# Kernel optimization log

Hardware: AMD Instinct MI355X
Metric: run time of the kernel (lower is better)

## Reference

```python
import jax, jax.numpy as jnp
import numpy as np

NEG_SLOPE = 0.2
EPS_SOFTMAX = 1e-16
EPS_NORM = 1e-12
H = 4


def gat_conv(x, src, dst, edge_attr, W, att_src, att_dst, W_edge, att_edge, bias, concat):
    """PyG GATConv with edge_dim, add_self_loops=False.
    x: [N, F_in]; src,dst: [E]; edge_attr: [E, edge_dim]
    W: [F_in, H*C]; att_src/att_dst/att_edge: [H, C]; W_edge: [edge_dim, H*C]
    """
    N = x.shape[0]
    C = att_src.shape[1]
    xs = (x @ W).reshape(N, H, C)                      # [N,H,C]
    a_s = jnp.einsum('nhc,hc->nh', xs, att_src)        # [N,H]
    a_d = jnp.einsum('nhc,hc->nh', xs, att_dst)        # [N,H]
    e = (edge_attr @ W_edge).reshape(-1, H, C)         # [E,H,C]
    a_e = jnp.einsum('ehc,hc->eh', e, att_edge)        # [E,H]
    alpha = a_s[src] + a_d[dst] + a_e                  # [E,H]
    alpha = jax.nn.leaky_relu(alpha, NEG_SLOPE)
    # segment softmax over edges grouped by destination node
    m = jax.ops.segment_max(alpha, dst, num_segments=N)        # [N,H]
    ex = jnp.exp(alpha - m[dst])
    denom = jax.ops.segment_sum(ex, dst, num_segments=N)       # [N,H]
    alpha = ex / (denom[dst] + EPS_SOFTMAX)
    # message = attention-weighted source features, scatter-add to dst
    out = jax.ops.segment_sum(xs[src] * alpha[..., None], dst, num_segments=N)  # [N,H,C]
    out = out.reshape(N, H * C) if concat else out.mean(axis=1)
    return out + bias


def l2_normalize(x):
    n = jnp.linalg.norm(x, axis=-1, keepdims=True)
    return x / jnp.maximum(n, EPS_NORM)


def setup_inputs() -> dict:
    key = jax.random.key(0)
    ks = jax.random.split(key, 16)
    N, E, F_in, C1, C2 = 50000, 800000, 128, 64, 64
    glorot = lambda k, shape: jax.random.uniform(
        k, shape, jnp.float32, -1.0, 1.0) * np.sqrt(6.0 / (shape[0] + shape[-1]))
    return {
        'x': jax.random.normal(ks[0], (N, F_in), jnp.float32),
        'edge_index': jax.random.randint(ks[1], (2, E), 0, N, jnp.int32),
        'edge_weight': jax.random.uniform(ks[2], (E, 1), jnp.float32),
        # layer 1: in=128 -> H*C1=256, concat=True
        'W1': glorot(ks[3], (F_in, H * C1)),
        'att_src1': glorot(ks[4], (H, C1)),
        'att_dst1': glorot(ks[5], (H, C1)),
        'We1': glorot(ks[6], (1, H * C1)),
        'att_e1': glorot(ks[7], (H, C1)),
        'b1': jnp.zeros((H * C1,), jnp.float32),
        # layer 2: in=256 -> H*C2, concat=False (mean over heads)
        'W2': glorot(ks[8], (H * C1, H * C2)),
        'att_src2': glorot(ks[9], (H, C2)),
        'att_dst2': glorot(ks[10], (H, C2)),
        'We2': glorot(ks[11], (1, H * C2)),
        'att_e2': glorot(ks[12], (H, C2)),
        'b2': jnp.zeros((C2,), jnp.float32),
    }


def reference(x, edge_index, edge_weight, W1, att_src1, att_dst1, We1, att_e1, b1,
              W2, att_src2, att_dst2, We2, att_e2, b2):
    src, dst = edge_index[0], edge_index[1]
    h = gat_conv(x, src, dst, edge_weight, W1, att_src1, att_dst1, We1, att_e1, b1, concat=True)
    h = jax.nn.relu(l2_normalize(h))
    out = gat_conv(h, src, dst, edge_weight, W2, att_src2, att_dst2, We2, att_e2, b2, concat=False)
    return out
```

## Files before the change

kernel.cpp:

```cpp
#include <hip/hip_runtime.h>
#include <hip/hip_bf16.h>

typedef unsigned short u16;
typedef unsigned long long u64;
using bf16x8 = __attribute__((ext_vector_type(8))) short;
using f32x4v = __attribute__((ext_vector_type(4))) float;
typedef float v2f __attribute__((ext_vector_type(2)));

#define HC 256
#define CDIM 64

__device__ __forceinline__ float b2f(u16 u){
  union { unsigned int i; float f; } c; c.i = ((unsigned)u) << 16; return c.f;
}
__device__ __forceinline__ u16 f2b(float f){
  union { float f; unsigned int i; } c; c.f = f;
  unsigned int x = c.i;
  return (u16)((x + 0x7FFFu + ((x >> 16) & 1u)) >> 16);
}
__device__ __forceinline__ float ldf(const void* p, size_t i, int isbf){
  return isbf ? b2f(((const u16*)p)[i]) : ((const float*)p)[i];
}
__device__ __forceinline__ float sel4(float4 v, int h){ return h==0?v.x:(h==1?v.y:(h==2?v.z:v.w)); }
__device__ __forceinline__ float lrelu(float v){ return v>0.f ? v : 0.2f*v; }

__device__ __forceinline__ void glds16(const void* g, void* l){
  __builtin_amdgcn_global_load_lds(
      (const __attribute__((address_space(1))) unsigned int*)g,
      (__attribute__((address_space(3))) unsigned int*)l, 16, 0, 0);
}

__device__ __forceinline__ float4 wave_max4(float4 m){
  #pragma unroll
  for(int o=32;o>0;o>>=1){
    m.x=fmaxf(m.x,__shfl_xor(m.x,o));
    m.y=fmaxf(m.y,__shfl_xor(m.y,o));
    m.z=fmaxf(m.z,__shfl_xor(m.z,o));
    m.w=fmaxf(m.w,__shfl_xor(m.w,o));
  }
  return m;
}
__device__ __forceinline__ float4 wave_sum4(float4 m){
  #pragma unroll
  for(int o=32;o>0;o>>=1){
    m.x+=__shfl_xor(m.x,o);
    m.y+=__shfl_xor(m.y,o);
    m.z+=__shfl_xor(m.z,o);
    m.w+=__shfl_xor(m.w,o);
  }
  return m;
}

__global__ void k_hist(const int* __restrict__ dst, int E, int N, int* __restrict__ deg,
                       int* __restrict__ rank,
                       const u16* __restrict__ x, int nelem, int* __restrict__ flag){
  int e = blockIdx.x*256 + threadIdx.x;
  if (e < E){
    int d = dst[e];
    if ((unsigned)d < (unsigned)N) rank[e] = atomicAdd(&deg[d], 1);
  }
  if (blockIdx.x == 0){
    __shared__ int bad;
    if (threadIdx.x==0) bad = 0;
    __syncthreads();
    int n = nelem < 8192 ? nelem : 8192;
    int localbad = 0;
    for (int i=threadIdx.x; i<n; i+=256){
      int ex = (x[i] >> 7) & 0xFF;
      if (ex >= 140) localbad++;
    }
    if (localbad) atomicAdd(&bad, 1);
    __syncthreads();
    if (threadIdx.x==0) *flag = (bad==0) ? 1 : 0;
  }
}

__global__ void k_scan1(const int* __restrict__ in, int* __restrict__ out, int* __restrict__ bsums, int n){
  __shared__ int s[256];
  int t = threadIdx.x;
  int i = blockIdx.x*256 + t;
  int v = (i<n)? in[i] : 0;
  s[t]=v; __syncthreads();
  for(int off=1; off<256; off<<=1){
    int tv = (t>=off)? s[t-off] : 0;
    __syncthreads();
    s[t]+=tv; __syncthreads();
  }
  if (i<n) out[i] = s[t]-v;
  if (t==255) bsums[blockIdx.x] = s[255];
}

__global__ void k_scan2(int* __restrict__ bsums, int nb){
  __shared__ int s[256];
  int t=threadIdx.x;
  int v=(t<nb)? bsums[t]:0;
  s[t]=v; __syncthreads();
  for(int off=1; off<256; off<<=1){
    int tv=(t>=off)? s[t-off]:0;
    __syncthreads();
    s[t]+=tv; __syncthreads();
  }
  if (t<nb) bsums[t]=s[t]-v;
}

__global__ void k_scatter(const int* __restrict__ src, const int* __restrict__ dst,
                          const void* __restrict__ ew, int E, int N,
                          const int* __restrict__ rowptr, const int* __restrict__ bsums,
                          const int* __restrict__ rank, u64* __restrict__ epk,
                          const int* __restrict__ flagp){
  int e = blockIdx.x*256+threadIdx.x;
  if (e>=E) return;
  int bf = *flagp;
  int d = dst[e];
  if ((unsigned)d >= (unsigned)N) return;
  int p = rowptr[d] + bsums[d>>8] + rank[e];
  int s = src[e];
  if ((unsigned)s >= (unsigned)N) s = 0;
  u64 v = ((u64)__float_as_uint(ldf(ew, e, bf)) << 32) | (unsigned)s;
  __builtin_nontemporal_store(v, &epk[p]);
}

__global__ void k_prep(const void* __restrict__ W1, const void* __restrict__ W2,
                       const void* __restrict__ We1, const void* __restrict__ ae1,
                       const void* __restrict__ We2, const void* __restrict__ ae2,
                       u16* __restrict__ Bt1, u16* __restrict__ Bt2, float* __restrict__ ce,
                       const int* __restrict__ flagp){
  int bf = *flagp;
  int b = blockIdx.x, t = threadIdx.x;
  if (b < 128){
    Bt1[(size_t)t*128 + b] = f2b(ldf(W1, (size_t)b*HC + t, bf));
  } else if (b < 384){
    int k = b - 128;
    Bt2[(size_t)t*256 + k] = f2b(ldf(W2, (size_t)k*HC + t, bf));
  } else {
    float p1 = ldf(We1, t, bf)*ldf(ae1, t, bf);
    float p2 = ldf(We2, t, bf)*ldf(ae2, t, bf);
    #pragma unroll
    for(int o=32;o>0;o>>=1){ p1+=__shfl_xor(p1,o); p2+=__shfl_xor(p2,o); }
    if((t&63)==0){ ce[t>>6]=p1; ce[4+(t>>6)]=p2; }
  }
}

__global__ __launch_bounds__(256) void k_gemm_mfma(
    const void* __restrict__ A, int a_ext, const u16* __restrict__ Bt,
    u16* __restrict__ C, const void* __restrict__ att_s, const void* __restrict__ att_d,
    float* __restrict__ a_s, float* __restrict__ a_d,
    int M, int K, const int* __restrict__ flagp)
{
  __shared__ u16 sh[64*264];
  __shared__ float att_sh[512];
  u16* As = sh;
  u16* Bs = sh + 2048;
  int bf = *flagp;
  int a_bf = a_ext ? bf : 1;
  int tid = threadIdx.x;
  int lane = tid & 63, w = tid >> 6;
  int quad = lane >> 4, ln = lane & 15;
  int m0 = blockIdx.x * 64;

  att_sh[tid]       = ldf(att_s, tid, bf);
  att_sh[256 + tid] = ldf(att_d, tid, bf);

  f32x4v acc[4][4] = {};
  for (int k0 = 0; k0 < K; k0 += 32){
    if (!a_ext){
      const u16* gA = (const u16*)A + (size_t)(m0 + (tid>>2))*K + k0 + (size_t)(tid&3)*8;
      glds16(gA, (char*)As + (size_t)w*1024);
    } else {
      int m = tid >> 2, g = tid & 3;
      int r = m0 + m;
      uint4 pack;
      if (r < M){
        size_t base = (size_t)r*K + k0 + g*8;
        if (a_bf){
          pack = *(const uint4*)((const u16*)A + base);
        } else {
          const float* Af = (const float*)A + base;
          float4 f0 = *(const float4*)Af;
          float4 f1 = *(const float4*)(Af+4);
          unsigned a0 = (unsigned)f2b(f0.x) | ((unsigned)f2b(f0.y)<<16);
          unsigned a1 = (unsigned)f2b(f0.z) | ((unsigned)f2b(f0.w)<<16);
          unsigned a2 = (unsigned)f2b(f1.x) | ((unsigned)f2b(f1.y)<<16);
          unsigned a3 = (unsigned)f2b(f1.z) | ((unsigned)f2b(f1.w)<<16);
          pack = make_uint4(a0,a1,a2,a3);
        }
      } else pack = make_uint4(0,0,0,0);
      ((uint4*)As)[tid] = pack;
    }
    #pragma unroll
    for (int i=0;i<4;i++){
      const u16* gB = Bt + (size_t)(i*64 + (tid>>2))*K + k0 + (size_t)(tid&3)*8;
      glds16(gB, (char*)Bs + (size_t)i*4096 + (size_t)w*1024);
    }
    __syncthreads();
    bf16x8 af[4], bfr[4];
    #pragma unroll
    for (int mi=0;mi<4;mi++) af[mi] = *(const bf16x8*)&As[(mi*16+ln)*32 + quad*8];
    #pragma unroll
    for (int nj=0;nj<4;nj++) bfr[nj] = *(const bf16x8*)&Bs[((size_t)w*64+nj*16+ln)*32 + quad*8];
    #pragma unroll
    for (int mi=0;mi<4;mi++)
      #pragma unroll
      for (int nj=0;nj<4;nj++)
        acc[mi][nj] = __builtin_amdgcn_mfma_f32_16x16x32_bf16(af[mi], bfr[nj], acc[mi][nj], 0,0,0);
    __syncthreads();
  }
  #pragma unroll
  for (int mi=0;mi<4;mi++)
    #pragma unroll
    for (int nj=0;nj<4;nj++){
      union { __hip_bfloat162 h2; u16 u[2]; } cv0, cv1;
      cv0.h2 = __float22bfloat162_rn(make_float2(acc[mi][nj][0], acc[mi][nj][1]));
      cv1.h2 = __float22bfloat162_rn(make_float2(acc[mi][nj][2], acc[mi][nj][3]));
      int col = w*64 + nj*16 + ln;
      int rbase = mi*16 + quad*4;
      sh[(rbase+0)*264 + col] = cv0.u[0];
      sh[(rbase+1)*264 + col] = cv0.u[1];
      sh[(rbase+2)*264 + col] = cv1.u[0];
      sh[(rbase+3)*264 + col] = cv1.u[1];
    }
  __syncthreads();
  #pragma unroll
  for (int j=0;j<8;j++){
    int idx = j*256 + tid;
    int r = idx >> 5, gq = idx & 31;
    if (m0 + r < M)
      *(uint4*)(C + (size_t)(m0+r)*HC + gq*8) = *(const uint4*)&sh[r*264 + gq*8];
  }
  {
    int r  = w*16 + ln;
    int hh = quad;
    const u16* crow = &sh[r*264 + hh*64];
    const float* asv = &att_sh[hh*64];
    const float* adv = &att_sh[256 + hh*64];
    float ps = 0.f, pd = 0.f;
    #pragma unroll
    for (int cb=0; cb<64; cb+=8){
      ushort4 ua = *(const ushort4*)&crow[cb];
      ushort4 ub = *(const ushort4*)&crow[cb+4];
      float4 sa = *(const float4*)&asv[cb];
      float4 sb = *(const float4*)&asv[cb+4];
      float4 da = *(const float4*)&adv[cb];
      float4 db = *(const float4*)&adv[cb+4];
      float c0=b2f(ua.x), c1=b2f(ua.y), c2=b2f(ua.z), c3=b2f(ua.w);
      float c4=b2f(ub.x), c5=b2f(ub.y), c6=b2f(ub.z), c7=b2f(ub.w);
      ps += c0*sa.x + c1*sa.y + c2*sa.z + c3*sa.w + c4*sb.x + c5*sb.y + c6*sb.z + c7*sb.w;
      pd += c0*da.x + c1*da.y + c2*da.z + c3*da.w + c4*db.x + c5*db.y + c6*db.z + c7*db.w;
    }
    if (m0 + r < M){
      a_s[(size_t)(m0+r)*4 + hh] = ps;
      a_d[(size_t)(m0+r)*4 + hh] = pd;
    }
  }
}

#define GRP4(E0, TWJ) { \
  int s0_=__builtin_amdgcn_readlane(s_reg,(E0)+0); \
  int s1_=__builtin_amdgcn_readlane(s_reg,(E0)+1); \
  int s2_=__builtin_amdgcn_readlane(s_reg,(E0)+2); \
  int s3_=__builtin_amdgcn_readlane(s_reg,(E0)+3); \
  uint2 x0_=*(const uint2*)&xs[(size_t)s0_*HC + (lane<<2)]; \
  uint2 x1_=*(const uint2*)&xs[(size_t)s1_*HC + (lane<<2)]; \
  uint2 x2_=*(const uint2*)&xs[(size_t)s2_*HC + (lane<<2)]; \
  uint2 x3_=*(const uint2*)&xs[(size_t)s3_*HC + (lane<<2)]; \
  float w0_=__shfl((TWJ), ibase+(((E0)+0)&15)); \
  float w1_=__shfl((TWJ), ibase+(((E0)+1)&15)); \
  float w2_=__shfl((TWJ), ibase+(((E0)+2)&15)); \
  float w3_=__shfl((TWJ), ibase+(((E0)+3)&15)); \
  v2f f_; \
  f_=(v2f){__uint_as_float(x0_.x<<16),__uint_as_float(x0_.x&0xFFFF0000u)}; a01+=f_*w0_; \
  f_=(v2f){__uint_as_float(x0_.y<<16),__uint_as_float(x0_.y&0xFFFF0000u)}; a23+=f_*w0_; \
  f_=(v2f){__uint_as_float(x1_.x<<16),__uint_as_float(x1_.x&0xFFFF0000u)}; a01+=f_*w1_; \
  f_=(v2f){__uint_as_float(x1_.y<<16),__uint_as_float(x1_.y&0xFFFF0000u)}; a23+=f_*w1_; \
  f_=(v2f){__uint_as_float(x2_.x<<16),__uint_as_float(x2_.x&0xFFFF0000u)}; a01+=f_*w2_; \
  f_=(v2f){__uint_as_float(x2_.y<<16),__uint_as_float(x2_.y&0xFFFF0000u)}; a23+=f_*w2_; \
  f_=(v2f){__uint_as_float(x3_.x<<16),__uint_as_float(x3_.x&0xFFFF0000u)}; a01+=f_*w3_; \
  f_=(v2f){__uint_as_float(x3_.y<<16),__uint_as_float(x3_.y&0xFFFF0000u)}; a23+=f_*w3_; \
}

__global__ __launch_bounds__(256) void k_soft_agg(
    const u16* __restrict__ xs, const int* __restrict__ rowptr, const int* __restrict__ bsums,
    const int* __restrict__ deg, const u64* __restrict__ epk,
    const float* __restrict__ a_s, const float* __restrict__ a_d, const float* __restrict__ ce4,
    const void* __restrict__ bias, void* __restrict__ outp, int N, int layer,
    const int* __restrict__ flagp){
  int bf = *flagp;
  int lane = threadIdx.x & 63;
  int w = threadIdx.x >> 6;
  int n = (blockIdx.x<<2) + w;
  if (n >= N) return;
  int row = rowptr[n] + bsums[n>>8];
  int dg = deg[n];
  float4 ad = *(const float4*)&a_d[(size_t)n*4];
  float4 ce = *(const float4*)ce4;
  int h = lane >> 4;
  float4 acc = make_float4(0.f,0.f,0.f,0.f);
  if (dg > 0){
    if (dg <= 64){
      u64 pk = 0;
      if (lane < dg) pk = epk[row + lane];
      int s = (int)(unsigned)(pk & 0xFFFFFFFFull);
      if ((unsigned)s >= (unsigned)N) s = 0;
      int s_reg = s;
      float wv = __uint_as_float((unsigned)(pk >> 32));
      float4 as4 = *(const float4*)&a_s[(size_t)s*4];
      uint2 xpf[8];
      #pragma unroll
      for (int k=0;k<8;k++){
        int sk = __builtin_amdgcn_readlane(s_reg, k);
        xpf[k] = *(const uint2*)&xs[(size_t)sk*HC + (lane<<2)];
      }
      bool vlane = lane < dg;
      float4 ex;
      ex.x = vlane ? __expf(lrelu(as4.x+ad.x+wv*ce.x)) : 0.f;
      ex.y = vlane ? __expf(lrelu(as4.y+ad.y+wv*ce.y)) : 0.f;
      ex.z = vlane ? __expf(lrelu(as4.z+ad.z+wv*ce.z)) : 0.f;
      ex.w = vlane ? __expf(lrelu(as4.w+ad.w+wv*ce.w)) : 0.f;
      float4 ss = ex;
      if (dg > 32){
        ss.x+=__shfl_xor(ss.x,32); ss.y+=__shfl_xor(ss.y,32);
        ss.z+=__shfl_xor(ss.z,32); ss.w+=__shfl_xor(ss.w,32);
      }
      if (dg > 16){
        ss.x+=__shfl_xor(ss.x,16); ss.y+=__shfl_xor(ss.y,16);
        ss.z+=__shfl_xor(ss.z,16); ss.w+=__shfl_xor(ss.w,16);
      }
      #pragma unroll
      for(int o=8;o>0;o>>=1){
        ss.x+=__shfl_xor(ss.x,o); ss.y+=__shfl_xor(ss.y,o);
        ss.z+=__shfl_xor(ss.z,o); ss.w+=__shfl_xor(ss.w,o);
      }
      float4 wgt;
      wgt.x = ex.x/(ss.x+1e-16f); wgt.y = ex.y/(ss.y+1e-16f);
      wgt.z = ex.z/(ss.z+1e-16f); wgt.w = ex.w/(ss.w+1e-16f);
      int ibase = lane & 48;
      float tw0, tw1, tw2, tw3;
      {
        int srcl = lane & 15;
        float c0=__shfl(wgt.x,srcl), c1=__shfl(wgt.y,srcl);
        float c2=__shfl(wgt.z,srcl), c3=__shfl(wgt.w,srcl);
        tw0 = (h==0)?c0:((h==1)?c1:((h==2)?c2:c3));
      }
      if (dg > 16){
        int srcl = 16 + (lane & 15);
        float c0=__shfl(wgt.x,srcl), c1=__shfl(wgt.y,srcl);
        float c2=__shfl(wgt.z,srcl), c3=__shfl(wgt.w,srcl);
        tw1 = (h==0)?c0:((h==1)?c1:((h==2)?c2:c3));
      } else tw1 = 0.f;
      if (dg > 32){
        int srcl = 32 + (lane & 15);
        float c0=__shfl(wgt.x,srcl), c1=__shfl(wgt.y,srcl);
        float c2=__shfl(wgt.z,srcl), c3=__shfl(wgt.w,srcl);
        tw2 = (h==0)?c0:((h==1)?c1:((h==2)?c2:c3));
      } else tw2 = 0.f;
      if (dg > 48){
        int srcl = 48 + (lane & 15);
        float c0=__shfl(wgt.x,srcl), c1=__shfl(wgt.y,srcl);
        float c2=__shfl(wgt.z,srcl), c3=__shfl(wgt.w,srcl);
        tw3 = (h==0)?c0:((h==1)?c1:((h==2)?c2:c3));
      } else tw3 = 0.f;
      v2f a01 = {0.f,0.f}, a23 = {0.f,0.f};
      #pragma unroll
      for (int k=0;k<8;k++){
        float wk = __shfl(tw0, ibase+k);
        uint2 xv = xpf[k];
        v2f f;
        f = (v2f){__uint_as_float(xv.x<<16), __uint_as_float(xv.x&0xFFFF0000u)}; a01 += f*wk;
        f = (v2f){__uint_as_float(xv.y<<16), __uint_as_float(xv.y&0xFFFF0000u)}; a23 += f*wk;
      }
      if (dg >  8) GRP4( 8, tw0);
      if (dg > 12) GRP4(12, tw0);
      if (dg > 16){
        GRP4(16, tw1);
        if (dg > 20) GRP4(20, tw1);
        if (dg > 24) GRP4(24, tw1);
        if (dg > 28) GRP4(28, tw1);
        if (dg > 32){
          GRP4(32, tw2);
          if (dg > 36) GRP4(36, tw2);
          if (dg > 40) GRP4(40, tw2);
          if (dg > 44) GRP4(44, tw2);
          if (dg > 48){
            GRP4(48, tw3);
            if (dg > 52) GRP4(52, tw3);
            if (dg > 56) GRP4(56, tw3);
            if (dg > 60) GRP4(60, tw3);
          }
        }
      }
      acc.x = a01.x; acc.y = a01.y; acc.z = a23.x; acc.w = a23.y;
    } else {
      float4 m = make_float4(-1e30f,-1e30f,-1e30f,-1e30f);
      for (int p=lane;p<dg;p+=64){
        u64 pk = epk[row+p];
        int s = (int)(unsigned)(pk & 0xFFFFFFFFull);
        if ((unsigned)s >= (unsigned)N) s = 0;
        float wv = __uint_as_float((unsigned)(pk >> 32));
        float4 as = *(const float4*)&a_s[(size_t)s*4];
        m.x=fmaxf(m.x, lrelu(as.x+ad.x+wv*ce.x));
        m.y=fmaxf(m.y, lrelu(as.y+ad.y+wv*ce.y));
        m.z=fmaxf(m.z, lrelu(as.z+ad.z+wv*ce.z));
        m.w=fmaxf(m.w, lrelu(as.w+ad.w+wv*ce.w));
      }
      m = wave_max4(m);
      float4 ss = make_float4(0.f,0.f,0.f,0.f);
      for (int p=lane;p<dg;p+=64){
        u64 pk = epk[row+p];
        int s = (int)(unsigned)(pk & 0xFFFFFFFFull);
        if ((unsigned)s >= (unsigned)N) s = 0;
        float wv = __uint_as_float((unsigned)(pk >> 32));
        float4 as = *(const float4*)&a_s[(size_t)s*4];
        ss.x+=__expf(lrelu(as.x+ad.x+wv*ce.x)-m.x);
        ss.y+=__expf(lrelu(as.y+ad.y+wv*ce.y)-m.y);
        ss.z+=__expf(lrelu(as.z+ad.z+wv*ce.z)-m.z);
        ss.w+=__expf(lrelu(as.w+ad.w+wv*ce.w)-m.w);
      }
      ss = wave_sum4(ss);
      float rsel=1.f/(sel4(ss,h)+1e-16f), mh=sel4(m,h), adh=sel4(ad,h), ceh=sel4(ce,h);
      for (int e=0;e<dg;e++){
        u64 pk = epk[row+e];
        int s = (int)(unsigned)(pk & 0xFFFFFFFFull);
        if ((unsigned)s >= (unsigned)N) s = 0;
        float wv = __uint_as_float((unsigned)(pk >> 32));
        float arv = lrelu(a_s[(size_t)s*4+h]+adh+wv*ceh);
        float wgt = __expf(arv-mh)*rsel;
        ushort4 xv4 = *(const ushort4*)&xs[(size_t)s*HC + lane*4];
        acc.x+=wgt*b2f(xv4.x); acc.y+=wgt*b2f(xv4.y);
        acc.z+=wgt*b2f(xv4.z); acc.w+=wgt*b2f(xv4.w);
      }
    }
  }
  if (layer==1){
    float4 v;
    v.x = acc.x + ldf(bias, lane*4+0, bf);
    v.y = acc.y + ldf(bias, lane*4+1, bf);
    v.z = acc.z + ldf(bias, lane*4+2, bf);
    v.w = acc.w + ldf(bias, lane*4+3, bf);
    float ss = v.x*v.x+v.y*v.y+v.z*v.z+v.w*v.w;
    #pragma unroll
    for(int o=32;o>0;o>>=1) ss += __shfl_xor(ss,o);
    float inv = 1.f/fmaxf(sqrtf(ss), 1e-12f);
    ushort4 o4;
    o4.x = f2b(fmaxf(v.x*inv,0.f)); o4.y = f2b(fmaxf(v.y*inv,0.f));
    o4.z = f2b(fmaxf(v.z*inv,0.f)); o4.w = f2b(fmaxf(v.w*inv,0.f));
    *(ushort4*)((u16*)outp + (size_t)n*HC + lane*4) = o4;
  } else {
    float4 s = acc;
    #pragma unroll
    for (int o=16;o<=32;o<<=1){
      s.x+=__shfl_xor(s.x,o); s.y+=__shfl_xor(s.y,o);
      s.z+=__shfl_xor(s.z,o); s.w+=__shfl_xor(s.w,o);
    }
    if (lane < 16){
      float4 v;
      v.x = 0.25f*s.x + ldf(bias, lane*4+0, bf);
      v.y = 0.25f*s.y + ldf(bias, lane*4+1, bf);
      v.z = 0.25f*s.z + ldf(bias, lane*4+2, bf);
      v.w = 0.25f*s.w + ldf(bias, lane*4+3, bf);
      if (bf){
        ushort4 o4; o4.x=f2b(v.x); o4.y=f2b(v.y); o4.z=f2b(v.z); o4.w=f2b(v.w);
        *(ushort4*)((u16*)outp + (size_t)n*CDIM + lane*4) = o4;
      } else {
        *(float4*)((float*)outp + (size_t)n*CDIM + lane*4) = v;
      }
    }
  }
}

extern "C" void kernel_launch(void* const* d_in, const int* in_sizes, int n_in,
                              void* d_out, int out_size, void* d_ws, size_t ws_size,
                              hipStream_t stream){
  const void* x_in = d_in[0];
  const int* eidx  = (const int*)d_in[1];
  const void* ew   = d_in[2];
  const void* W1   = d_in[3];
  const void* as1  = d_in[4];
  const void* ad1  = d_in[5];
  const void* We1  = d_in[6];
  const void* ae1  = d_in[7];
  const void* b1   = d_in[8];
  const void* W2   = d_in[9];
  const void* as2  = d_in[10];
  const void* ad2  = d_in[11];
  const void* We2  = d_in[12];
  const void* ae2  = d_in[13];
  const void* b2   = d_in[14];

  int N = in_sizes[0]/128;
  int E = in_sizes[2];
  const int* src = eidx;
  const int* dst = eidx + E;

  char* w = (char*)d_ws;
  auto alloc = [&](size_t bytes)->char*{ char* p=w; w += (bytes+255)/256*256; return p; };
  int*   flag  = (int*)alloc(256);
  u16*   xs    = (u16*)alloc((size_t)N*HC*2);
  u16*   agg   = (u16*)alloc((size_t)N*HC*2);
  float* a_s   = (float*)alloc((size_t)N*4*4);
  float* a_d   = (float*)alloc((size_t)N*4*4);
  int*   deg   = (int*)alloc((size_t)N*4);
  int*   rowptr= (int*)alloc((size_t)N*4);
  int*   bsums = (int*)alloc(256*4);
  int*   rank  = (int*)alloc((size_t)E*4);
  u64*   epk   = (u64*)alloc((size_t)E*8);
  float* ce    = (float*)alloc(256);
  u16*   Bt1   = (u16*)alloc((size_t)HC*128*2);
  u16*   Bt2   = (u16*)alloc((size_t)HC*HC*2);

  (void)hipMemsetAsync(deg, 0, (size_t)N*4, stream);

  int eb = (E+255)/256;
  int nb = (N+255)/256;
  k_hist<<<eb,256,0,stream>>>(dst, E, N, deg, rank, (const u16*)x_in, in_sizes[0], flag);
  k_scan1<<<nb,256,0,stream>>>(deg, rowptr, bsums, N);
  k_scan2<<<1,256,0,stream>>>(bsums, nb);
  k_scatter<<<eb,256,0,stream>>>(src, dst, ew, E, N, rowptr, bsums, rank, epk, flag);
  k_prep<<<385,256,0,stream>>>(W1, W2, We1, ae1, We2, ae2, Bt1, Bt2, ce, flag);

  int gemmBlocks = (N+63)/64;
  int nwb = (N+3)/4;

  k_gemm_mfma<<<gemmBlocks,256,0,stream>>>(x_in, 1, Bt1, xs, as1, ad1, a_s, a_d, N, 128, flag);
  k_soft_agg<<<nwb,256,0,stream>>>(xs, rowptr, bsums, deg, epk, a_s, a_d, ce, b1, agg, N, 1, flag);

  k_gemm_mfma<<<gemmBlocks,256,0,stream>>>(agg, 0, Bt2, xs, as2, ad2, a_s, a_d, N, 256, flag);
  k_soft_agg<<<nwb,256,0,stream>>>(xs, rowptr, bsums, deg, epk, a_s, a_d, ce+4, b2, d_out, N, 2, flag);
}
```

Before: 328.5 us.

## Merge prep into histogram and scatter into layer-1 GEMM launches; widen prefetch

The weight-transpose/prep kernel is folded into the histogram launch as extra blocks, with each prep block recomputing the bf16 flag locally. The edge scatter is likewise folded into the first GEMM launch as extra blocks, which removes two kernel launches and lets independent work overlap. The GEMM now uses the direct global-to-LDS load path for bf16 external input on full tiles. The aggregation kernel prefetches 16 neighbor rows instead of 8 before consuming them. The cost is more registers in aggregation and a heterogeneous block mix within the fused launches.

```diff
diff --git a/kernel.cpp b/kernel.cpp
--- a/kernel.cpp
+++ b/kernel.cpp
@@ -51,27 +51,64 @@
   return m;
 }
 
-__global__ void k_hist(const int* __restrict__ dst, int E, int N, int* __restrict__ deg,
-                       int* __restrict__ rank,
-                       const u16* __restrict__ x, int nelem, int* __restrict__ flag){
-  int e = blockIdx.x*256 + threadIdx.x;
-  if (e < E){
-    int d = dst[e];
-    if ((unsigned)d < (unsigned)N) rank[e] = atomicAdd(&deg[d], 1);
-  }
-  if (blockIdx.x == 0){
-    __shared__ int bad;
-    if (threadIdx.x==0) bad = 0;
-    __syncthreads();
+__global__ __launch_bounds__(256) void k_hist_prep(
+    const int* __restrict__ dst, int E, int N, int* __restrict__ deg,
+    int* __restrict__ rank,
+    const u16* __restrict__ x, int nelem, int* __restrict__ flag,
+    const void* __restrict__ W1, const void* __restrict__ W2,
+    const void* __restrict__ We1, const void* __restrict__ ae1,
+    const void* __restrict__ We2, const void* __restrict__ ae2,
+    u16* __restrict__ Bt1, u16* __restrict__ Bt2, float* __restrict__ ce){
+  int eb = (E + 255) >> 8;
+  int t = threadIdx.x;
+  if ((int)blockIdx.x < eb){
+    int e = blockIdx.x*256 + t;
+    if (e < E){
+      int d = dst[e];
+      if ((unsigned)d < (unsigned)N) rank[e] = atomicAdd(&deg[d], 1);
+    }
+    if (blockIdx.x == 0){
+      __shared__ int bad0;
+      if (t==0) bad0 = 0;
+      __syncthreads();
+      int n = nelem < 8192 ? nelem : 8192;
+      int lb = 0;
+      for (int i=t; i<n; i+=256){
+        int ex = (x[i] >> 7) & 0xFF;
+        if (ex >= 140) lb++;
+      }
+      if (lb) atomicAdd(&bad0, 1);
+      __syncthreads();
+      if (t==0) *flag = (bad0==0) ? 1 : 0;
+    }
+    return;
+  }
+  __shared__ int bad;
+  if (t==0) bad = 0;
+  __syncthreads();
+  {
     int n = nelem < 8192 ? nelem : 8192;
-    int localbad = 0;
-    for (int i=threadIdx.x; i<n; i+=256){
+    int lb = 0;
+    for (int i=t; i<n; i+=256){
       int ex = (x[i] >> 7) & 0xFF;
-      if (ex >= 140) localbad++;
-    }
-    if (localbad) atomicAdd(&bad, 1);
-    __syncthreads();
-    if (threadIdx.x==0) *flag = (bad==0) ? 1 : 0;
+      if (ex >= 140) lb++;
+    }
+    if (lb) atomicAdd(&bad, 1);
+  }
+  __syncthreads();
+  int bf = (bad==0) ? 1 : 0;
+  int b = blockIdx.x - eb;
+  if (b < 128){
+    Bt1[(size_t)t*128 + b] = f2b(ldf(W1, (size_t)b*HC + t, bf));
+  } else if (b < 384){
+    int k = b - 128;
+    Bt2[(size_t)t*256 + k] = f2b(ldf(W2, (size_t)k*HC + t, bf));
+  } else {
+    float p1 = ldf(We1, t, bf)*ldf(ae1, t, bf);
+    float p2 = ldf(We2, t, bf)*ldf(ae2, t, bf);
+    #pragma unroll
+    for(int o=32;o>0;o>>=1){ p1+=__shfl_xor(p1,o); p2+=__shfl_xor(p2,o); }
+    if((t&63)==0){ ce[t>>6]=p1; ce[4+(t>>6)]=p2; }
   }
 }
 
@@ -103,67 +140,44 @@
   if (t<nb) bsums[t]=s[t]-v;
 }
 
-__global__ void k_scatter(const int* __restrict__ src, const int* __restrict__ dst,
-                          const void* __restrict__ ew, int E, int N,
-                          const int* __restrict__ rowptr, const int* __restrict__ bsums,
-                          const int* __restrict__ rank, u64* __restrict__ epk,
-                          const int* __restrict__ flagp){
-  int e = blockIdx.x*256+threadIdx.x;
+__device__ __forceinline__ void scatter_body(int sb, const int* __restrict__ srcv,
+    const int* __restrict__ dst, const void* __restrict__ ew, int E, int N,
+    const int* __restrict__ rowptr, const int* __restrict__ bsums, const int* __restrict__ rank,
+    u64* __restrict__ epk, int bf){
+  int e = sb*256 + threadIdx.x;
   if (e>=E) return;
-  int bf = *flagp;
   int d = dst[e];
   if ((unsigned)d >= (unsigned)N) return;
   int p = rowptr[d] + bsums[d>>8] + rank[e];
-  int s = src[e];
+  int s = srcv[e];
   if ((unsigned)s >= (unsigned)N) s = 0;
   u64 v = ((u64)__float_as_uint(ldf(ew, e, bf)) << 32) | (unsigned)s;
   __builtin_nontemporal_store(v, &epk[p]);
 }
 
-__global__ void k_prep(const void* __restrict__ W1, const void* __restrict__ W2,
-                       const void* __restrict__ We1, const void* __restrict__ ae1,
-                       const void* __restrict__ We2, const void* __restrict__ ae2,
-                       u16* __restrict__ Bt1, u16* __restrict__ Bt2, float* __restrict__ ce,
-                       const int* __restrict__ flagp){
-  int bf = *flagp;
-  int b = blockIdx.x, t = threadIdx.x;
-  if (b < 128){
-    Bt1[(size_t)t*128 + b] = f2b(ldf(W1, (size_t)b*HC + t, bf));
-  } else if (b < 384){
-    int k = b - 128;
-    Bt2[(size_t)t*256 + k] = f2b(ldf(W2, (size_t)k*HC + t, bf));
-  } else {
-    float p1 = ldf(We1, t, bf)*ldf(ae1, t, bf);
-    float p2 = ldf(We2, t, bf)*ldf(ae2, t, bf);
-    #pragma unroll
-    for(int o=32;o>0;o>>=1){ p1+=__shfl_xor(p1,o); p2+=__shfl_xor(p2,o); }
-    if((t&63)==0){ ce[t>>6]=p1; ce[4+(t>>6)]=p2; }
-  }
-}
-
-__global__ __launch_bounds__(256) void k_gemm_mfma(
+__device__ __forceinline__ void gemm_body(int bidx,
     const void* __restrict__ A, int a_ext, const u16* __restrict__ Bt,
     u16* __restrict__ C, const void* __restrict__ att_s, const void* __restrict__ att_d,
     float* __restrict__ a_s, float* __restrict__ a_d,
-    int M, int K, const int* __restrict__ flagp)
+    int M, int K, int bf)
 {
   __shared__ u16 sh[64*264];
   __shared__ float att_sh[512];
   u16* As = sh;
   u16* Bs = sh + 2048;
-  int bf = *flagp;
   int a_bf = a_ext ? bf : 1;
   int tid = threadIdx.x;
   int lane = tid & 63, w = tid >> 6;
   int quad = lane >> 4, ln = lane & 15;
-  int m0 = blockIdx.x * 64;
+  int m0 = bidx * 64;
+  bool adma = (!a_ext) || (a_bf && (m0 + 64 <= M));
 
   att_sh[tid]       = ldf(att_s, tid, bf);
   att_sh[256 + tid] = ldf(att_d, tid, bf);
 
   f32x4v acc[4][4] = {};
   for (int k0 = 0; k0 < K; k0 += 32){
-    if (!a_ext){
+    if (adma){
       const u16* gA = (const u16*)A + (size_t)(m0 + (tid>>2))*K + k0 + (size_t)(tid&3)*8;
       glds16(gA, (char*)As + (size_t)w*1024);
     } else {
@@ -251,6 +265,30 @@
       a_s[(size_t)(m0+r)*4 + hh] = ps;
       a_d[(size_t)(m0+r)*4 + hh] = pd;
     }
+  }
+}
+
+__global__ __launch_bounds__(256) void k_gemm_mfma(
+    const void* __restrict__ A, int a_ext, const u16* __restrict__ Bt,
+    u16* __restrict__ C, const void* __restrict__ att_s, const void* __restrict__ att_d,
+    float* __restrict__ a_s, float* __restrict__ a_d,
+    int M, int K, const int* __restrict__ flagp){
+  gemm_body(blockIdx.x, A, a_ext, Bt, C, att_s, att_d, a_s, a_d, M, K, *flagp);
+}
+
+__global__ __launch_bounds__(256) void k_gemm_scatter(
+    const void* __restrict__ A, const u16* __restrict__ Bt,
+    u16* __restrict__ C, const void* __restrict__ att_s, const void* __restrict__ att_d,
+    float* __restrict__ a_s, float* __restrict__ a_d,
+    int M, int K, const int* __restrict__ flagp, int gemmBlocks,
+    const int* __restrict__ srcv, const int* __restrict__ dst, const void* __restrict__ ew,
+    int E, const int* __restrict__ rowptr, const int* __restrict__ bsums,
+    const int* __restrict__ rank, u64* __restrict__ epk){
+  int bf = *flagp;
+  if ((int)blockIdx.x < gemmBlocks){
+    gemm_body(blockIdx.x, A, 1, Bt, C, att_s, att_d, a_s, a_d, M, K, bf);
+  } else {
+    scatter_body(blockIdx.x - gemmBlocks, srcv, dst, ew, E, M, rowptr, bsums, rank, epk, bf);
   }
 }
 
@@ -304,9 +342,9 @@
       int s_reg = s;
       float wv = __uint_as_float((unsigned)(pk >> 32));
       float4 as4 = *(const float4*)&a_s[(size_t)s*4];
-      uint2 xpf[8];
+      uint2 xpf[16];
       #pragma unroll
-      for (int k=0;k<8;k++){
+      for (int k=0;k<16;k++){
         int sk = __builtin_amdgcn_readlane(s_reg, k);
         xpf[k] = *(const uint2*)&xs[(size_t)sk*HC + (lane<<2)];
       }
@@ -361,15 +399,13 @@
       } else tw3 = 0.f;
       v2f a01 = {0.f,0.f}, a23 = {0.f,0.f};
       #pragma unroll
-      for (int k=0;k<8;k++){
+      for (int k=0;k<16;k++){
         float wk = __shfl(tw0, ibase+k);
         uint2 xv = xpf[k];
         v2f f;
         f = (v2f){__uint_as_float(xv.x<<16), __uint_as_float(xv.x&0xFFFF0000u)}; a01 += f*wk;
         f = (v2f){__uint_as_float(xv.y<<16), __uint_as_float(xv.y&0xFFFF0000u)}; a23 += f*wk;
       }
-      if (dg >  8) GRP4( 8, tw0);
-      if (dg > 12) GRP4(12, tw0);
       if (dg > 16){
         GRP4(16, tw1);
         if (dg > 20) GRP4(20, tw1);
@@ -488,14 +524,14 @@
 
   int N = in_sizes[0]/128;
   int E = in_sizes[2];
-  const int* src = eidx;
-  const int* dst = eidx + E;
+  const int* srcp = eidx;
+  const int* dstp = eidx + E;
 
   char* w = (char*)d_ws;
   auto alloc = [&](size_t bytes)->char*{ char* p=w; w += (bytes+255)/256*256; return p; };
   int*   flag  = (int*)alloc(256);
   u16*   xs    = (u16*)alloc((size_t)N*HC*2);
-  u16*   agg   = (u16*)alloc((size_t)N*HC*2);
+  u16*   hbuf  = (u16*)alloc((size_t)N*HC*2);
   float* a_s   = (float*)alloc((size_t)N*4*4);
   float* a_d   = (float*)alloc((size_t)N*4*4);
   int*   deg   = (int*)alloc((size_t)N*4);
@@ -511,18 +547,19 @@
 
   int eb = (E+255)/256;
   int nb = (N+255)/256;
-  k_hist<<<eb,256,0,stream>>>(dst, E, N, deg, rank, (const u16*)x_in, in_sizes[0], flag);
+  int nelem = in_sizes[0];
+  k_hist_prep<<<eb+385,256,0,stream>>>(dstp, E, N, deg, rank, (const u16*)x_in, nelem, flag,
+                                       W1, W2, We1, ae1, We2, ae2, Bt1, Bt2, ce);
   k_scan1<<<nb,256,0,stream>>>(deg, rowptr, bsums, N);
   k_scan2<<<1,256,0,stream>>>(bsums, nb);
-  k_scatter<<<eb,256,0,stream>>>(src, dst, ew, E, N, rowptr, bsums, rank, epk, flag);
-  k_prep<<<385,256,0,stream>>>(W1, W2, We1, ae1, We2, ae2, Bt1, Bt2, ce, flag);
 
   int gemmBlocks = (N+63)/64;
   int nwb = (N+3)/4;
 
-  k_gemm_mfma<<<gemmBlocks,256,0,stream>>>(x_in, 1, Bt1, xs, as1, ad1, a_s, a_d, N, 128, flag);
-  k_soft_agg<<<nwb,256,0,stream>>>(xs, rowptr, bsums, deg, epk, a_s, a_d, ce, b1, agg, N, 1, flag);
-
-  k_gemm_mfma<<<gemmBlocks,256,0,stream>>>(agg, 0, Bt2, xs, as2, ad2, a_s, a_d, N, 256, flag);
+  k_gemm_scatter<<<gemmBlocks+eb,256,0,stream>>>(x_in, Bt1, xs, as1, ad1, a_s, a_d, N, 128, flag,
+                                                 gemmBlocks, srcp, dstp, ew, E, rowptr, bsums, rank, epk);
+  k_soft_agg<<<nwb,256,0,stream>>>(xs, rowptr, bsums, deg, epk, a_s, a_d, ce, b1, hbuf, N, 1, flag);
+
+  k_gemm_mfma<<<gemmBlocks,256,0,stream>>>(hbuf, 0, Bt2, xs, as2, ad2, a_s, a_d, N, 256, flag);
   k_soft_agg<<<nwb,256,0,stream>>>(xs, rowptr, bsums, deg, epk, a_s, a_d, ce+4, b2, d_out, N, 2, flag);
 }
```

Measured after the change: 316.0 us. -3.8%, faster.
